# Kernel tuning notes

Hardware: AMD Instinct MI355X
Metric: run time of the kernel (lower is better)

Reference implementation:

```python
import jax, jax.numpy as jnp
import numpy as np

N = 100000          # nodes
E = 3200000         # edges
C_IN = 64
HIDDEN = 64
NUM_CLASSES = 10
NUM_GRAPHS = 256
EPS = 1e-5


def _graph_conv(x, src, dst, w_rel, w_root, b):
    # PyG GraphConv(aggr='mean'): out_i = W_rel * mean_{j->i} x_j + W_root * x_i + b
    msg_sum = jax.ops.segment_sum(x[src], dst, num_segments=N)            # [N, C]
    cnt = jax.ops.segment_sum(jnp.ones((src.shape[0], 1), x.dtype), dst,
                              num_segments=N)                             # [N, 1]
    agg = msg_sum / jnp.maximum(cnt, 1.0)
    return agg @ w_rel + x @ w_root + b


def _batch_norm(x, gamma, beta):
    # PyG BatchNorm in training mode: batch stats over the node dimension
    mean = jnp.mean(x, axis=0)
    var = jnp.var(x, axis=0)
    return (x - mean) * jax.lax.rsqrt(var + EPS) * gamma + beta


def setup_inputs() -> dict:
    key = jax.random.key(0)
    ks = jax.random.split(key, 20)
    x = jax.random.normal(ks[0], (N, C_IN), dtype=jnp.float32)
    edge_index = jax.random.randint(ks[1], (2, E), 0, N, dtype=jnp.int32)
    batch = jnp.sort(jax.random.randint(ks[2], (N,), 0, NUM_GRAPHS, dtype=jnp.int32))

    def lin(k, fan_in, fan_out):
        s = 1.0 / np.sqrt(fan_in)
        return jax.random.uniform(k, (fan_in, fan_out), jnp.float32, -s, s)

    dims = [(C_IN, 16), (16, 32), (32, 32), (32, HIDDEN)]
    params = {}
    ki = 3
    for i, (ci, co) in enumerate(dims, start=1):
        params[f"w_rel{i}"] = lin(ks[ki], ci, co); ki += 1
        params[f"w_root{i}"] = lin(ks[ki], ci, co); ki += 1
        params[f"b{i}"] = jnp.zeros((co,), jnp.float32)
        params[f"g{i}"] = jnp.ones((co,), jnp.float32)
        params[f"be{i}"] = jnp.zeros((co,), jnp.float32)
    params["w_lin1"] = lin(ks[ki], HIDDEN, HIDDEN); ki += 1
    params["b_lin1"] = jnp.zeros((HIDDEN,), jnp.float32)
    params["w_lin2"] = lin(ks[ki], HIDDEN, NUM_CLASSES); ki += 1
    params["b_lin2"] = jnp.zeros((NUM_CLASSES,), jnp.float32)

    return {"x": x, "edge_index": edge_index, "batch": batch, **params}


def reference(x, edge_index, batch,
              w_rel1, w_root1, b1, g1, be1,
              w_rel2, w_root2, b2, g2, be2,
              w_rel3, w_root3, b3, g3, be3,
              w_rel4, w_root4, b4, g4, be4,
              w_lin1, b_lin1, w_lin2, b_lin2):
    src, dst = edge_index[0], edge_index[1]
    h = jax.nn.elu(_batch_norm(_graph_conv(x, src, dst, w_rel1, w_root1, b1), g1, be1))
    h = jax.nn.elu(_batch_norm(_graph_conv(h, src, dst, w_rel2, w_root2, b2), g2, be2))
    h = jax.nn.elu(_batch_norm(_graph_conv(h, src, dst, w_rel3, w_root3, b3), g3, be3))
    h = jax.nn.elu(_batch_norm(_graph_conv(h, src, dst, w_rel4, w_root4, b4), g4, be4))
    # global mean pool over graphs
    pooled = jax.ops.segment_sum(h, batch, num_segments=NUM_GRAPHS)
    cnt = jax.ops.segment_sum(jnp.ones((N, 1), h.dtype), batch, num_segments=NUM_GRAPHS)
    pooled = pooled / jnp.maximum(cnt, 1.0)
    z = jax.nn.relu(pooled @ w_lin1 + b_lin1)
    # dropout omitted (deterministic / eval mode)
    logits = z @ w_lin2 + b_lin2
    return jax.nn.log_softmax(logits, axis=-1)
```

## Files before the change

### kernel.cpp

```cpp
#include <hip/hip_runtime.h>
#include <hip/hip_bf16.h>
#include <math.h>

#define NGRAPHS 256
#define BSHIFT 8
#define NBUCK 512
#define NSORT 256
#define LSTAT 2048
#define GCHUNK 1024
#define SMASK 0x00FFFFFFu

__device__ __forceinline__ float bf2f(unsigned short u) {
    return __uint_as_float((unsigned)u << 16);
}
__device__ __forceinline__ unsigned short f2bf(float f) {
    unsigned u = __float_as_uint(f);
    unsigned r = (u + 0x7FFFu + ((u >> 16) & 1u)) >> 16;
    return (unsigned short)r;
}

__global__ __launch_bounds__(256) void k_bhist(const int* __restrict__ dst, int* __restrict__ hmat, int E,
                                               const float* __restrict__ x, const float* __restrict__ w_rel1,
                                               unsigned short* __restrict__ y1b,
                                               int* __restrict__ colpos, int N) {
    int bid = blockIdx.x, tid = threadIdx.x;
    if (bid < NSORT) {
        __shared__ int hist[NBUCK];
        for (int i = tid; i < NBUCK; i += 256) hist[i] = 0;
        __syncthreads();
        int chunk = (E + NSORT - 1) / NSORT;
        int lo = bid * chunk;
        int hi = lo + chunk; if (hi > E) hi = E;
        for (int i = lo + tid; i < hi; i += 256)
            atomicAdd(&hist[__builtin_nontemporal_load(dst + i) >> BSHIFT], 1);
        __syncthreads();
        for (int i = tid; i < NBUCK; i += 256) {
            int h = hist[i];
            int base = atomicAdd(&colpos[i], h);
            hmat[(size_t)bid * NBUCK + i] = base;
        }
    } else {
        __shared__ float s_rel[64 * 16];
        for (int i = tid; i < 64 * 16; i += 256) s_rel[i] = w_rel1[i];
        __syncthreads();
        int total = N * 4;
        int nb = gridDim.x - NSORT;
        for (int i = (bid - NSORT) * 256 + tid; i < total; i += nb * 256) {
            int n = i >> 2, c0 = (i & 3) << 2;
            const float4* mp = (const float4*)(x + (size_t)n * 64);
            float4 acc; acc.x = 0.f; acc.y = 0.f; acc.z = 0.f; acc.w = 0.f;
#pragma unroll
            for (int k2 = 0; k2 < 16; k2++) {
                float4 v = mp[k2];
                const float* wr = &s_rel[(k2 * 4) * 16 + c0];
                float4 w0 = *(const float4*)(wr);
                float4 w1 = *(const float4*)(wr + 16);
                float4 w2 = *(const float4*)(wr + 32);
                float4 w3 = *(const float4*)(wr + 48);
                acc.x += v.x * w0.x + v.y * w1.x + v.z * w2.x + v.w * w3.x;
                acc.y += v.x * w0.y + v.y * w1.y + v.z * w2.y + v.w * w3.y;
                acc.z += v.x * w0.z + v.y * w1.z + v.z * w2.z + v.w * w3.z;
                acc.w += v.x * w0.w + v.y * w1.w + v.z * w2.w + v.w * w3.w;
            }
            ushort4 o; o.x = f2bf(acc.x); o.y = f2bf(acc.y); o.z = f2bf(acc.z); o.w = f2bf(acc.w);
            *(ushort4*)(y1b + (size_t)n * 16 + c0) = o;
        }
    }
}

__global__ __launch_bounds__(512) void k_bscatter(const int* __restrict__ src, const int* __restrict__ dst,
                                                  const int* __restrict__ hmat, const int* __restrict__ colpos,
                                                  int* __restrict__ bstart_g,
                                                  unsigned* __restrict__ ebuf, int E) {
    __shared__ int s[NBUCK];
    __shared__ int cur[NBUCK];
    int tid = threadIdx.x;
    int b = blockIdx.x;
    int v = colpos[tid];
    s[tid] = v;
    __syncthreads();
    for (int off = 1; off < NBUCK; off <<= 1) {
        int t = (tid >= off) ? s[tid - off] : 0;
        __syncthreads();
        s[tid] += t;
        __syncthreads();
    }
    int excl = s[tid] - v;
    if (b == 0) {
        bstart_g[tid] = excl;
        if (tid == NBUCK - 1) bstart_g[NBUCK] = s[NBUCK - 1];
    }
    cur[tid] = excl + hmat[(size_t)b * NBUCK + tid];
    __syncthreads();
    int chunk = (E + NSORT - 1) / NSORT;
    int lo = b * chunk;
    int hi = lo + chunk; if (hi > E) hi = E;
    for (int i = lo + tid; i < hi; i += 512) {
        int d = __builtin_nontemporal_load(dst + i);
        int sv = __builtin_nontemporal_load(src + i);
        int p = atomicAdd(&cur[d >> BSHIFT], 1);
        ebuf[p] = (unsigned)sv | ((unsigned)(d & 255) << 24);
    }
}

__global__ __launch_bounds__(256) void k_sort2(const unsigned* __restrict__ ebuf, const int* __restrict__ bstart,
                                               int* __restrict__ csr, int* __restrict__ row_start, int N) {
    __shared__ int hist[256];
    __shared__ int sc[256];
    __shared__ int scur[256];
    int b = blockIdx.x;
    int e0 = bstart[b], e1 = bstart[b + 1];
    hist[threadIdx.x] = 0;
    __syncthreads();
    for (int i = e0 + threadIdx.x; i < e1; i += 256)
        atomicAdd(&hist[__builtin_nontemporal_load(ebuf + i) >> 24], 1);
    __syncthreads();
    sc[threadIdx.x] = hist[threadIdx.x];
    __syncthreads();
    for (int off = 1; off < 256; off <<= 1) {
        int t = (threadIdx.x >= off) ? sc[threadIdx.x - off] : 0;
        __syncthreads();
        sc[threadIdx.x] += t;
        __syncthreads();
    }
    {
        int inc = sc[threadIdx.x];
        int ex = inc - hist[threadIdx.x];
        scur[threadIdx.x] = e0 + ex;
        int node = (b << BSHIFT) + threadIdx.x;
        if (node < N) row_start[node] = e0 + ex;
        if (node == N - 1) row_start[N] = e0 + inc;
    }
    __syncthreads();
    for (int i = e0 + threadIdx.x; i < e1; i += 256) {
        unsigned w = __builtin_nontemporal_load(ebuf + i);
        int p = atomicAdd(&scur[w >> 24], 1);
        csr[p] = (int)(w & SMASK);
    }
}

template <int C>
__global__ __launch_bounds__(256) void k_gather(const unsigned short* __restrict__ h,
                                                const int* __restrict__ row_start,
                                                const int* __restrict__ csr, float* __restrict__ agg, int N) {
    constexpr int LPR = C / 4;
    constexpr int EPP = 64 / LPR;
    constexpr int BATCH = 4 * EPP;
    __shared__ int sbuf[GCHUNK];
    int lane = threadIdx.x & 63;
    int w = threadIdx.x >> 6;
    int nb = blockIdx.x * 4;
    int wid = nb + w;
    bool act = wid < N;
    int nb_end = nb + 4; if (nb_end > N) nb_end = N;
    int eb0 = row_start[nb];
    int eb1 = row_start[nb_end];
    int r0 = act ? row_start[wid] : 0;
    int r1 = act ? row_start[wid + 1] : 0;
    int es = lane / LPR;
    int cq = (lane % LPR) * 4;

    float a0 = 0.f, a1 = 0.f, a2 = 0.f, a3 = 0.f;
    for (int base = eb0; base < eb1; base += GCHUNK) {
        int len = eb1 - base; if (len > GCHUNK) len = GCHUNK;
        __syncthreads();
        for (int i = threadIdx.x; i < len; i += 256)
            sbuf[i] = __builtin_nontemporal_load(csr + base + i);
        __syncthreads();
        if (act) {
            int lo = (r0 > base ? r0 : base) - base;
            int hiv = r1 < base + len ? r1 : base + len;
            int hi = hiv - base;
            for (int j0 = lo; j0 < hi; j0 += BATCH) {
                int s[4]; bool p[4];
#pragma unroll
                for (int u = 0; u < 4; u++) {
                    int j = j0 + u * EPP + es;
                    p[u] = j < hi;
                    s[u] = sbuf[p[u] ? j : j0];
                }
                ushort4 v[4];
#pragma unroll
                for (int u = 0; u < 4; u++)
                    v[u] = *(const ushort4*)(h + (size_t)s[u] * C + cq);
#pragma unroll
                for (int u = 0; u < 4; u++) {
                    if (p[u]) {
                        a0 += bf2f(v[u].x); a1 += bf2f(v[u].y);
                        a2 += bf2f(v[u].z); a3 += bf2f(v[u].w);
                    }
                }
            }
        }
    }
#pragma unroll
    for (int off = LPR; off < 64; off <<= 1) {
        a0 += __shfl_xor(a0, off, 64);
        a1 += __shfl_xor(a1, off, 64);
        a2 += __shfl_xor(a2, off, 64);
        a3 += __shfl_xor(a3, off, 64);
    }
    if (act && lane < LPR) {
        int deg = r1 - r0;
        float rec = 1.0f / (float)(deg > 0 ? deg : 1);
        float4 o; o.x = a0 * rec; o.y = a1 * rec; o.z = a2 * rec; o.w = a3 * rec;
        *(float4*)(agg + (size_t)wid * C + cq) = o;
    }
}

template <int CI, int CO, bool HAS_REL, bool ADD_AGG, bool IN_BF16>
__global__ __launch_bounds__(256) void k_lin_stats(const void* __restrict__ hroot_v, const float* __restrict__ hrel,
                                                   const float* __restrict__ w_rel, const float* __restrict__ w_root,
                                                   const float* __restrict__ bias,
                                                   float* __restrict__ out, float* __restrict__ gsl, int N) {
    constexpr int QPR = CO / 4;
    __shared__ float s_rel[HAS_REL ? CI * CO : 1];
    __shared__ float s_root[CI * CO];
    __shared__ float s_b[CO];
    __shared__ float part[4][2 * CO];
    int tid = threadIdx.x;
    if (HAS_REL)
        for (int i = tid; i < CI * CO; i += 256) s_rel[i] = w_rel[i];
    for (int i = tid; i < CI * CO; i += 256) s_root[i] = w_root[i];
    if (tid < CO) s_b[tid] = bias[tid];
    __syncthreads();

    int total = N * QPR;
    int stride = gridDim.x * 256;
    float s0 = 0, s1 = 0, s2 = 0, s3 = 0, q0 = 0, q1 = 0, q2 = 0, q3 = 0;
    for (int i = blockIdx.x * 256 + tid; i < total; i += stride) {
        int n = i / QPR, c0 = (i % QPR) * 4;
        float4 acc = *(const float4*)&s_b[c0];
        if (ADD_AGG) {
            float4 v = ((const float4*)hrel)[i];
            acc.x += v.x; acc.y += v.y; acc.z += v.z; acc.w += v.w;
        }
#pragma unroll
        for (int cb = 0; cb < CI / 4; cb++) {
            float f0, f1, f2, f3;
            if (IN_BF16) {
                ushort4 v = *(const ushort4*)((const unsigned short*)hroot_v + (size_t)n * CI + cb * 4);
                f0 = bf2f(v.x); f1 = bf2f(v.y); f2 = bf2f(v.z); f3 = bf2f(v.w);
            } else {
                float4 v = *(const float4*)((const float*)hroot_v + (size_t)n * CI + cb * 4);
                f0 = v.x; f1 = v.y; f2 = v.z; f3 = v.w;
            }
            const float* wr = &s_root[(cb * 4) * CO + c0];
            float4 w0 = *(const float4*)(wr);
            float4 w1 = *(const float4*)(wr + CO);
            float4 w2 = *(const float4*)(wr + 2 * CO);
            float4 w3 = *(const float4*)(wr + 3 * CO);
            acc.x += f0 * w0.x + f1 * w1.x + f2 * w2.x + f3 * w3.x;
            acc.y += f0 * w0.y + f1 * w1.y + f2 * w2.y + f3 * w3.y;
            acc.z += f0 * w0.z + f1 * w1.z + f2 * w2.z + f3 * w3.z;
            acc.w += f0 * w0.w + f1 * w1.w + f2 * w2.w + f3 * w3.w;
            if (HAS_REL) {
                float4 a = *(const float4*)(hrel + (size_t)n * CI + cb * 4);
                const float* we = &s_rel[(cb * 4) * CO + c0];
                float4 e0 = *(const float4*)(we);
                float4 e1 = *(const float4*)(we + CO);
                float4 e2 = *(const float4*)(we + 2 * CO);
                float4 e3 = *(const float4*)(we + 3 * CO);
                acc.x += a.x * e0.x + a.y * e1.x + a.z * e2.x + a.w * e3.x;
                acc.y += a.x * e0.y + a.y * e1.y + a.z * e2.y + a.w * e3.y;
                acc.z += a.x * e0.z + a.y * e1.z + a.z * e2.z + a.w * e3.z;
                acc.w += a.x * e0.w + a.y * e1.w + a.z * e2.w + a.w * e3.w;
            }
        }
        ((float4*)out)[i] = acc;
        s0 += acc.x; q0 += acc.x * acc.x;
        s1 += acc.y; q1 += acc.y * acc.y;
        s2 += acc.z; q2 += acc.z * acc.z;
        s3 += acc.w; q3 += acc.w * acc.w;
    }
#pragma unroll
    for (int off = QPR; off < 64; off <<= 1) {
        s0 += __shfl_xor(s0, off, 64); q0 += __shfl_xor(q0, off, 64);
        s1 += __shfl_xor(s1, off, 64); q1 += __shfl_xor(q1, off, 64);
        s2 += __shfl_xor(s2, off, 64); q2 += __shfl_xor(q2, off, 64);
        s3 += __shfl_xor(s3, off, 64); q3 += __shfl_xor(q3, off, 64);
    }
    int lane = tid & 63;
    int w = tid >> 6;
    if (lane < QPR) {
        int cq = lane * 4;
        part[w][cq + 0] = s0; part[w][CO + cq + 0] = q0;
        part[w][cq + 1] = s1; part[w][CO + cq + 1] = q1;
        part[w][cq + 2] = s2; part[w][CO + cq + 2] = q2;
        part[w][cq + 3] = s3; part[w][CO + cq + 3] = q3;
    }
    __syncthreads();
    if (tid < 2 * CO) {
        float v = part[0][tid] + part[1][tid] + part[2][tid] + part[3][tid];
        atomicAdd(&gsl[tid], v);
    }
}

template <int CO>
__global__ __launch_bounds__(256) void k_bn_elu(const float* __restrict__ h, const float* __restrict__ gsl,
                                                const float* __restrict__ g, const float* __restrict__ be,
                                                unsigned short* __restrict__ hb, float invN, int N) {
    __shared__ float sc[CO], sh[CO];
    if (threadIdx.x < CO) {
        int c = threadIdx.x;
        float mean = gsl[c] * invN;
        float var = gsl[CO + c] * invN - mean * mean;
        float s = g[c] * rsqrtf(var + 1e-5f);
        sc[c] = s;
        sh[c] = be[c] - mean * s;
    }
    __syncthreads();
    int total = N * (CO / 4);
    int i = blockIdx.x * 256 + threadIdx.x;
    if (i >= total) return;
    float4 v = ((const float4*)h)[i];
    int cq = (i % (CO / 4)) * 4;
    v.x = v.x * sc[cq + 0] + sh[cq + 0];
    v.y = v.y * sc[cq + 1] + sh[cq + 1];
    v.z = v.z * sc[cq + 2] + sh[cq + 2];
    v.w = v.w * sc[cq + 3] + sh[cq + 3];
    v.x = v.x > 0.f ? v.x : expm1f(v.x);
    v.y = v.y > 0.f ? v.y : expm1f(v.y);
    v.z = v.z > 0.f ? v.z : expm1f(v.z);
    v.w = v.w > 0.f ? v.w : expm1f(v.w);
    ushort4 o;
    o.x = f2bf(v.x); o.y = f2bf(v.y); o.z = f2bf(v.z); o.w = f2bf(v.w);
    ((ushort4*)hb)[i] = o;
}

__global__ __launch_bounds__(256) void k_bn_elu_pool(const float* __restrict__ h, const float* __restrict__ gsl,
                                                     const float* __restrict__ g, const float* __restrict__ be,
                                                     const int* __restrict__ batch,
                                                     float* __restrict__ pooled, float* __restrict__ cntg,
                                                     float invN, int N) {
    __shared__ float sc[64], sh[64];
    if (threadIdx.x < 64) {
        int c = threadIdx.x;
        float mean = gsl[c] * invN;
        float var = gsl[64 + c] * invN - mean * mean;
        float s = g[c] * rsqrtf(var + 1e-5f);
        sc[c] = s;
        sh[c] = be[c] - mean * s;
    }
    __syncthreads();
    int lane = threadIdx.x & 63;
    int wid = blockIdx.x * 4 + (threadIdx.x >> 6);
    int n0 = wid * 16;
    if (n0 >= N) return;
    float scl = sc[lane];
    float shl = sh[lane];
    int nmax = N - n0; if (nmax > 16) nmax = 16;
    int cur = batch[n0];
    float acc = 0.f;
    float run = 0.f;
    for (int k = 0; k < nmax; k++) {
        int gg = batch[n0 + k];
        if (gg != cur) {
            atomicAdd(&pooled[(size_t)cur * 64 + lane], acc);
            if (lane == 0) atomicAdd(&cntg[cur], run);
            cur = gg; acc = 0.f; run = 0.f;
        }
        float v = h[(size_t)(n0 + k) * 64 + lane] * scl + shl;
        v = v > 0.f ? v : expm1f(v);
        acc += v;
        run += 1.f;
    }
    atomicAdd(&pooled[(size_t)cur * 64 + lane], acc);
    if (lane == 0) atomicAdd(&cntg[cur], run);
}

__global__ __launch_bounds__(256) void k_head(const float* __restrict__ pooled, const float* __restrict__ cntg,
                                              const float* __restrict__ w1, const float* __restrict__ b1,
                                              const float* __restrict__ w2, const float* __restrict__ b2,
                                              float* __restrict__ out) {
    int g = threadIdx.x;
    float rec = 1.0f / fmaxf(cntg[g], 1.0f);
    float p[64];
    {
        const float4* pp = (const float4*)(pooled + (size_t)g * 64);
#pragma unroll
        for (int i = 0; i < 16; i++) {
            float4 v = pp[i];
            p[4 * i + 0] = v.x * rec; p[4 * i + 1] = v.y * rec;
            p[4 * i + 2] = v.z * rec; p[4 * i + 3] = v.w * rec;
        }
    }
    float lg[10];
#pragma unroll
    for (int t = 0; t < 10; t++) lg[t] = b2[t];
#pragma unroll 1
    for (int j = 0; j < 64; j++) {
        float a = b1[j];
#pragma unroll
        for (int k = 0; k < 64; k++) a += p[k] * w1[k * 64 + j];
        a = fmaxf(a, 0.f);
#pragma unroll
        for (int t = 0; t < 10; t++) lg[t] += a * w2[j * 10 + t];
    }
    float m = -1e30f;
#pragma unroll
    for (int t = 0; t < 10; t++) m = fmaxf(m, lg[t]);
    float s = 0.f;
#pragma unroll
    for (int t = 0; t < 10; t++) s += expf(lg[t] - m);
    float lse = m + logf(s);
#pragma unroll
    for (int t = 0; t < 10; t++) out[(size_t)g * 10 + t] = lg[t] - lse;
}

extern "C" void kernel_launch(void* const* d_in, const int* in_sizes, int n_in,
                              void* d_out, int out_size, void* d_ws, size_t ws_size,
                              hipStream_t stream) {
    const float* x = (const float*)d_in[0];
    const int* ei = (const int*)d_in[1];
    const int* batch = (const int*)d_in[2];
    const int N = in_sizes[0] / 64;
    const int E = in_sizes[1] / 2;
    const int* src = ei;
    const int* dst = ei + E;

    const float* w_rel1 = (const float*)d_in[3];
    const float* w_root1 = (const float*)d_in[4];
    const float* b1 = (const float*)d_in[5];
    const float* g1 = (const float*)d_in[6];
    const float* be1 = (const float*)d_in[7];
    const float* w_rel2 = (const float*)d_in[8];
    const float* w_root2 = (const float*)d_in[9];
    const float* b2 = (const float*)d_in[10];
    const float* g2 = (const float*)d_in[11];
    const float* be2 = (const float*)d_in[12];
    const float* w_rel3 = (const float*)d_in[13];
    const float* w_root3 = (const float*)d_in[14];
    const float* b3 = (const float*)d_in[15];
    const float* g3 = (const float*)d_in[16];
    const float* be3 = (const float*)d_in[17];
    const float* w_rel4 = (const float*)d_in[18];
    const float* w_root4 = (const float*)d_in[19];
    const float* b4 = (const float*)d_in[20];
    const float* g4 = (const float*)d_in[21];
    const float* be4 = (const float*)d_in[22];
    const float* w_lin1 = (const float*)d_in[23];
    const float* b_lin1 = (const float*)d_in[24];
    const float* w_lin2 = (const float*)d_in[25];
    const float* b_lin2 = (const float*)d_in[26];

    char* ws = (char*)d_ws;
    size_t off = 0;
    auto alloc = [&](size_t bytes) { size_t o = off; off += (bytes + 255) & ~(size_t)255; return o; };
    int* hmat = (int*)(ws + alloc((size_t)NSORT * NBUCK * 4));
    int* bstart = (int*)(ws + alloc((size_t)(NBUCK + 1) * 4));
    unsigned* ebuf = (unsigned*)(ws + alloc((size_t)E * 4));
    int* csr = (int*)(ws + alloc((size_t)E * 4));
    int* row_start = (int*)(ws + alloc((size_t)(N + 1) * 4));
    float* agg = (float*)(ws + alloc((size_t)N * 32 * 4));
    unsigned short* y1b = (unsigned short*)(ws + alloc((size_t)N * 16 * 2));
    unsigned short* hb = (unsigned short*)(ws + alloc((size_t)N * 64 * 2));
    float* bufA = (float*)(ws + alloc((size_t)N * 64 * 4));
    const int zwords = NBUCK + 512 + NGRAPHS * 64 + NGRAPHS;
    int* colpos = (int*)(ws + alloc((size_t)zwords * 4));
    float* gs = (float*)(colpos + NBUCK);
    float* pooled = gs + 512;
    float* cntg = pooled + NGRAPHS * 64;

    hipMemsetAsync(colpos, 0, (size_t)zwords * 4, stream);

    const float invN = 1.0f / (float)N;
    const int gbl = (N + 3) / 4;

    k_bhist<<<1024, 256, 0, stream>>>(dst, hmat, E, x, w_rel1, y1b, colpos, N);
    k_bscatter<<<NSORT, 512, 0, stream>>>(src, dst, hmat, colpos, bstart, ebuf, E);
    k_sort2<<<NBUCK, 256, 0, stream>>>(ebuf, bstart, csr, row_start, N);

    k_gather<16><<<gbl, 256, 0, stream>>>(y1b, row_start, csr, agg, N);
    k_lin_stats<64, 16, false, true, false><<<LSTAT, 256, 0, stream>>>(
        x, agg, nullptr, w_root1, b1, bufA, gs + 0, N);
    k_bn_elu<16><<<(N * 4 + 255) / 256, 256, 0, stream>>>(bufA, gs + 0, g1, be1, hb, invN, N);

    k_gather<16><<<gbl, 256, 0, stream>>>(hb, row_start, csr, agg, N);
    k_lin_stats<16, 32, true, false, true><<<LSTAT, 256, 0, stream>>>(
        hb, agg, w_rel2, w_root2, b2, bufA, gs + 128, N);
    k_bn_elu<32><<<(N * 8 + 255) / 256, 256, 0, stream>>>(bufA, gs + 128, g2, be2, hb, invN, N);

    k_gather<32><<<gbl, 256, 0, stream>>>(hb, row_start, csr, agg, N);
    k_lin_stats<32, 32, true, false, true><<<LSTAT, 256, 0, stream>>>(
        hb, agg, w_rel3, w_root3, b3, bufA, gs + 256, N);
    k_bn_elu<32><<<(N * 8 + 255) / 256, 256, 0, stream>>>(bufA, gs + 256, g3, be3, hb, invN, N);

    k_gather<32><<<gbl, 256, 0, stream>>>(hb, row_start, csr, agg, N);
    k_lin_stats<32, 64, true, false, true><<<LSTAT, 256, 0, stream>>>(
        hb, agg, w_rel4, w_root4, b4, bufA, gs + 384, N);
    int waves16 = (N + 15) / 16;
    k_bn_elu_pool<<<(waves16 + 3) / 4, 256, 0, stream>>>(
        bufA, gs + 384, g4, be4, batch, pooled, cntg, invN, N);

    k_head<<<1, 256, 0, stream>>>(pooled, cntg, w_lin1, b_lin1, w_lin2, b_lin2, (float*)d_out);
}
```

Before: 658.0 us.

## Hold linear weights in registers with one output channel per lane

The linear+stats kernel now gives each lane a single output channel and keeps that channel's weight column in registers, instead of staging the weight matrices in shared memory and computing four channels per thread. This removes shared-memory weight reads and the staging barrier. In exchange, each lane of a node group reads the same input row (broadcast loads), and the register count grows with CI. The persistent grid is halved to 1024 blocks.

```diff
diff --git a/kernel.cpp b/kernel.cpp
--- a/kernel.cpp
+++ b/kernel.cpp
@@ -6,7 +6,7 @@
 #define BSHIFT 8
 #define NBUCK 512
 #define NSORT 256
-#define LSTAT 2048
+#define LGRID 1024
 #define GCHUNK 1024
 #define SMASK 0x00FFFFFFu
 
@@ -213,82 +213,61 @@
                                                    const float* __restrict__ w_rel, const float* __restrict__ w_root,
                                                    const float* __restrict__ bias,
                                                    float* __restrict__ out, float* __restrict__ gsl, int N) {
-    constexpr int QPR = CO / 4;
-    __shared__ float s_rel[HAS_REL ? CI * CO : 1];
-    __shared__ float s_root[CI * CO];
-    __shared__ float s_b[CO];
+    constexpr int NPW = 64 / CO;
     __shared__ float part[4][2 * CO];
     int tid = threadIdx.x;
-    if (HAS_REL)
-        for (int i = tid; i < CI * CO; i += 256) s_rel[i] = w_rel[i];
-    for (int i = tid; i < CI * CO; i += 256) s_root[i] = w_root[i];
-    if (tid < CO) s_b[tid] = bias[tid];
-    __syncthreads();
-
-    int total = N * QPR;
-    int stride = gridDim.x * 256;
-    float s0 = 0, s1 = 0, s2 = 0, s3 = 0, q0 = 0, q1 = 0, q2 = 0, q3 = 0;
-    for (int i = blockIdx.x * 256 + tid; i < total; i += stride) {
-        int n = i / QPR, c0 = (i % QPR) * 4;
-        float4 acc = *(const float4*)&s_b[c0];
-        if (ADD_AGG) {
-            float4 v = ((const float4*)hrel)[i];
-            acc.x += v.x; acc.y += v.y; acc.z += v.z; acc.w += v.w;
-        }
-#pragma unroll
-        for (int cb = 0; cb < CI / 4; cb++) {
-            float f0, f1, f2, f3;
-            if (IN_BF16) {
-                ushort4 v = *(const ushort4*)((const unsigned short*)hroot_v + (size_t)n * CI + cb * 4);
-                f0 = bf2f(v.x); f1 = bf2f(v.y); f2 = bf2f(v.z); f3 = bf2f(v.w);
-            } else {
-                float4 v = *(const float4*)((const float*)hroot_v + (size_t)n * CI + cb * 4);
-                f0 = v.x; f1 = v.y; f2 = v.z; f3 = v.w;
-            }
-            const float* wr = &s_root[(cb * 4) * CO + c0];
-            float4 w0 = *(const float4*)(wr);
-            float4 w1 = *(const float4*)(wr + CO);
-            float4 w2 = *(const float4*)(wr + 2 * CO);
-            float4 w3 = *(const float4*)(wr + 3 * CO);
-            acc.x += f0 * w0.x + f1 * w1.x + f2 * w2.x + f3 * w3.x;
-            acc.y += f0 * w0.y + f1 * w1.y + f2 * w2.y + f3 * w3.y;
-            acc.z += f0 * w0.z + f1 * w1.z + f2 * w2.z + f3 * w3.z;
-            acc.w += f0 * w0.w + f1 * w1.w + f2 * w2.w + f3 * w3.w;
-            if (HAS_REL) {
-                float4 a = *(const float4*)(hrel + (size_t)n * CI + cb * 4);
-                const float* we = &s_rel[(cb * 4) * CO + c0];
-                float4 e0 = *(const float4*)(we);
-                float4 e1 = *(const float4*)(we + CO);
-                float4 e2 = *(const float4*)(we + 2 * CO);
-                float4 e3 = *(const float4*)(we + 3 * CO);
-                acc.x += a.x * e0.x + a.y * e1.x + a.z * e2.x + a.w * e3.x;
-                acc.y += a.x * e0.y + a.y * e1.y + a.z * e2.y + a.w * e3.y;
-                acc.z += a.x * e0.z + a.y * e1.z + a.z * e2.z + a.w * e3.z;
-                acc.w += a.x * e0.w + a.y * e1.w + a.z * e2.w + a.w * e3.w;
-            }
-        }
-        ((float4*)out)[i] = acc;
-        s0 += acc.x; q0 += acc.x * acc.x;
-        s1 += acc.y; q1 += acc.y * acc.y;
-        s2 += acc.z; q2 += acc.z * acc.z;
-        s3 += acc.w; q3 += acc.w * acc.w;
-    }
-#pragma unroll
-    for (int off = QPR; off < 64; off <<= 1) {
-        s0 += __shfl_xor(s0, off, 64); q0 += __shfl_xor(q0, off, 64);
-        s1 += __shfl_xor(s1, off, 64); q1 += __shfl_xor(q1, off, 64);
-        s2 += __shfl_xor(s2, off, 64); q2 += __shfl_xor(q2, off, 64);
-        s3 += __shfl_xor(s3, off, 64); q3 += __shfl_xor(q3, off, 64);
-    }
     int lane = tid & 63;
     int w = tid >> 6;
-    if (lane < QPR) {
-        int cq = lane * 4;
-        part[w][cq + 0] = s0; part[w][CO + cq + 0] = q0;
-        part[w][cq + 1] = s1; part[w][CO + cq + 1] = q1;
-        part[w][cq + 2] = s2; part[w][CO + cq + 2] = q2;
-        part[w][cq + 3] = s3; part[w][CO + cq + 3] = q3;
-    }
+    int ch = lane % CO;
+    int sub = lane / CO;
+
+    float wro[CI];
+#pragma unroll
+    for (int ci = 0; ci < CI; ci++) wro[ci] = w_root[ci * CO + ch];
+    float wre[HAS_REL ? CI : 1];
+    if (HAS_REL) {
+#pragma unroll
+        for (int ci = 0; ci < CI; ci++) wre[ci] = w_rel[ci * CO + ch];
+    }
+    float bch = bias[ch];
+
+    int ngrp = (N + NPW - 1) / NPW;
+    int gw = blockIdx.x * 4 + w;
+    int nwv = gridDim.x * 4;
+    float ssum = 0.f, qsum = 0.f;
+    for (int g = gw; g < ngrp; g += nwv) {
+        int n = g * NPW + sub;
+        if (n < N) {
+            float acc = bch;
+            if (ADD_AGG) acc += hrel[(size_t)n * CO + ch];
+#pragma unroll
+            for (int cb = 0; cb < CI / 4; cb++) {
+                float f0, f1, f2, f3;
+                if (IN_BF16) {
+                    ushort4 v = *(const ushort4*)((const unsigned short*)hroot_v + (size_t)n * CI + cb * 4);
+                    f0 = bf2f(v.x); f1 = bf2f(v.y); f2 = bf2f(v.z); f3 = bf2f(v.w);
+                } else {
+                    float4 v = *(const float4*)((const float*)hroot_v + (size_t)n * CI + cb * 4);
+                    f0 = v.x; f1 = v.y; f2 = v.z; f3 = v.w;
+                }
+                acc += f0 * wro[cb * 4 + 0] + f1 * wro[cb * 4 + 1]
+                     + f2 * wro[cb * 4 + 2] + f3 * wro[cb * 4 + 3];
+                if (HAS_REL) {
+                    float4 a = *(const float4*)(hrel + (size_t)n * CI + cb * 4);
+                    acc += a.x * wre[cb * 4 + 0] + a.y * wre[cb * 4 + 1]
+                         + a.z * wre[cb * 4 + 2] + a.w * wre[cb * 4 + 3];
+                }
+            }
+            out[(size_t)n * CO + ch] = acc;
+            ssum += acc; qsum += acc * acc;
+        }
+    }
+#pragma unroll
+    for (int off = CO; off < 64; off <<= 1) {
+        ssum += __shfl_xor(ssum, off, 64);
+        qsum += __shfl_xor(qsum, off, 64);
+    }
+    if (lane < CO) { part[w][lane] = ssum; part[w][CO + lane] = qsum; }
     __syncthreads();
     if (tid < 2 * CO) {
         float v = part[0][tid] + part[1][tid] + part[2][tid] + part[3][tid];
@@ -472,22 +451,22 @@
     k_sort2<<<NBUCK, 256, 0, stream>>>(ebuf, bstart, csr, row_start, N);
 
     k_gather<16><<<gbl, 256, 0, stream>>>(y1b, row_start, csr, agg, N);
-    k_lin_stats<64, 16, false, true, false><<<LSTAT, 256, 0, stream>>>(
+    k_lin_stats<64, 16, false, true, false><<<LGRID, 256, 0, stream>>>(
         x, agg, nullptr, w_root1, b1, bufA, gs + 0, N);
     k_bn_elu<16><<<(N * 4 + 255) / 256, 256, 0, stream>>>(bufA, gs + 0, g1, be1, hb, invN, N);
 
     k_gather<16><<<gbl, 256, 0, stream>>>(hb, row_start, csr, agg, N);
-    k_lin_stats<16, 32, true, false, true><<<LSTAT, 256, 0, stream>>>(
+    k_lin_stats<16, 32, true, false, true><<<LGRID, 256, 0, stream>>>(
         hb, agg, w_rel2, w_root2, b2, bufA, gs + 128, N);
     k_bn_elu<32><<<(N * 8 + 255) / 256, 256, 0, stream>>>(bufA, gs + 128, g2, be2, hb, invN, N);
 
     k_gather<32><<<gbl, 256, 0, stream>>>(hb, row_start, csr, agg, N);
-    k_lin_stats<32, 32, true, false, true><<<LSTAT, 256, 0, stream>>>(
+    k_lin_stats<32, 32, true, false, true><<<LGRID, 256, 0, stream>>>(
         hb, agg, w_rel3, w_root3, b3, bufA, gs + 256, N);
     k_bn_elu<32><<<(N * 8 + 255) / 256, 256, 0, stream>>>(bufA, gs + 256, g3, be3, hb, invN, N);
 
     k_gather<32><<<gbl, 256, 0, stream>>>(hb, row_start, csr, agg, N);
-    k_lin_stats<32, 64, true, false, true><<<LSTAT, 256, 0, stream>>>(
+    k_lin_stats<32, 64, true, false, true><<<LGRID, 256, 0, stream>>>(
         hb, agg, w_rel4, w_root4, b4, bufA, gs + 384, N);
     int waves16 = (N + 15) / 16;
     k_bn_elu_pool<<<(waves16 + 3) / 4, 256, 0, stream>>>(
```

New measurement: 616.4 us. 1.07x faster.
